# Performance work log

Measured on AMD Instinct MI355X. Metric: run time of the kernel, lower is better.

## Reference

```python
import jax, jax.numpy as jnp
import numpy as np

K = 3  # dynamic kernel size


def _conv(x, w, b, pad):
    # x: [B,Cin,H,W], w: [Cout,Cin,kh,kw]
    y = jax.lax.conv_general_dilated(
        x, w, window_strides=(1, 1), padding=pad,
        dimension_numbers=("NCHW", "OIHW", "NCHW"))
    return y + b[None, :, None, None]


def setup_inputs() -> dict:
    key = jax.random.key(0)
    ks = jax.random.split(key, 9)
    B, C, H, W = 16, 256, 64, 64
    sc1 = 1.0 / np.sqrt(C * 9)
    sc3 = 1.0 / np.sqrt(C)
    return {
        "x":    jax.random.normal(ks[0], (B, C, H, W), jnp.float32),
        "kin":  jax.random.normal(ks[1], (B, C, H, W), jnp.float32),
        "w1":   jax.random.normal(ks[2], (C, C, 3, 3), jnp.float32) * sc1,
        "b1":   jax.random.normal(ks[3], (C,), jnp.float32) * 0.01,
        "w2":   jax.random.normal(ks[4], (C, C, 3, 3), jnp.float32) * sc1,
        "b2":   jax.random.normal(ks[5], (C,), jnp.float32) * 0.01,
        "w3":   jax.random.normal(ks[6], (K * K * C, C, 1, 1), jnp.float32) * sc3,
        "b3":   jax.random.normal(ks[7], (K * K * C,), jnp.float32) * 0.01,
        "bias": jax.random.normal(ks[8], (C,), jnp.float32) * 0.01,
    }


def reference(x, kin, w1, b1, w2, b2, w3, b3, bias):
    B, C, H, W = x.shape
    # tokernel: conv3x3 (valid) -> lrelu(0.1) -> conv3x3 -> lrelu -> global avg pool -> 1x1 conv
    h = jax.nn.leaky_relu(_conv(kin, w1, b1, "VALID"), 0.1)
    h = jax.nn.leaky_relu(_conv(h, w2, b2, "VALID"), 0.1)
    p = h.mean(axis=(2, 3))                                   # [B,C] adaptive avg pool 1x1
    kern = jnp.einsum("bc,oc->bo", p, w3.reshape(K * K * C, C)) + b3  # 1x1 conv
    kern = kern.reshape(B, C, 1, K, K)                        # per-sample depthwise weights

    pad = [(K // 2, K // 2)] * 2

    def dw(xi, wi):  # xi: [C,H,W], wi: [C,1,K,K]
        return jax.lax.conv_general_dilated(
            xi[None], wi, window_strides=(1, 1), padding=pad,
            dimension_numbers=("NCHW", "OIHW", "NCHW"),
            feature_group_count=C)[0]

    y = jax.vmap(dw)(x, kern)                                 # [B,C,H,W]
    return y + bias[None, :, None, None]
```

## Files before the change

kernel.cpp:

```cpp
#include <hip/hip_runtime.h>
#include <hip/hip_bf16.h>
#include <stdint.h>

#define CCH 256

typedef __attribute__((ext_vector_type(8))) short short8;
typedef __attribute__((ext_vector_type(4))) float f32x4;

__device__ __forceinline__ float lrelu(float v) { return v > 0.f ? v : 0.1f * v; }

__device__ __forceinline__ unsigned short f2bf(float f) {
    __hip_bfloat16 h = __float2bfloat16(f);
    return *reinterpret_cast<unsigned short*>(&h);
}

__device__ __forceinline__ void gl_lds16(const void* g, void* s) {
    __builtin_amdgcn_global_load_lds(
        (const __attribute__((address_space(1))) unsigned int*)(uintptr_t)g,
        (__attribute__((address_space(3))) unsigned int*)(unsigned int)(uintptr_t)s,
        16, 0, 0);
}

__device__ __forceinline__ void pipe_barrier() {
    asm volatile("" ::: "memory");
    __builtin_amdgcn_s_barrier();
    asm volatile("" ::: "memory");
}

__global__ __launch_bounds__(256)
void nhwc_k(const float* __restrict__ in, unsigned short* __restrict__ out)
{
    __shared__ float t[32][65];
    const int tid = threadIdx.x;
    const int kc = blockIdx.x, y = blockIdx.y, b = blockIdx.z;
    const float* src = in + ((size_t)(b * 256 + kc * 32)) * 4096 + y * 64;
#pragma unroll
    for (int i = 0; i < 2; ++i) {
        int idx = tid + i * 256;
        int cl = idx >> 4, xg = idx & 15;
        float4 v = *(const float4*)(src + (size_t)cl * 4096 + xg * 4);
        t[cl][xg * 4 + 0] = v.x; t[cl][xg * 4 + 1] = v.y;
        t[cl][xg * 4 + 2] = v.z; t[cl][xg * 4 + 3] = v.w;
    }
    __syncthreads();
    const int x = tid >> 2, cg = tid & 3;
    union { unsigned short us[8]; uint4 v; } u;
#pragma unroll
    for (int j = 0; j < 8; ++j) u.us[j] = f2bf(t[cg * 8 + j][x]);
    unsigned short* dst = out + (((size_t)(b * 8 + kc) * 4096 + y * 64 + x) * 32 + cg * 8);
    *(uint4*)dst = u.v;
}

__global__ __launch_bounds__(256)
void wtr_k(const float* __restrict__ w1, const float* __restrict__ w2,
           unsigned short* __restrict__ o1, unsigned short* __restrict__ o2)
{
    const int kc = blockIdx.x / 9, t = blockIdx.x - kc * 9;
    const float* w = blockIdx.y ? w2 : w1;
    unsigned short* o = blockIdx.y ? o2 : o1;
    const int co = threadIdx.x;
#pragma unroll
    for (int q = 0; q < 4; ++q) {
        union { unsigned short us[8]; uint4 v; } u;
#pragma unroll
        for (int uu = 0; uu < 8; ++uu)
            u.us[uu] = f2bf(w[((size_t)co * 256 + kc * 32 + q * 8 + uu) * 9 + t]);
        *(uint4*)(o + ((size_t)((kc * 9 + t) * 4 + q)) * 2048 + co * 8) = u.v;
    }
}

__global__ __launch_bounds__(256)
void zero_pool_k(float* __restrict__ p) { p[blockIdx.x * 256 + threadIdx.x] = 0.f; }

template<int POOL, int WIN, int WOUT>
__global__ __launch_bounds__(256, 2)
void convmm_k(const unsigned short* __restrict__ im, const unsigned short* __restrict__ wt,
              const float* __restrict__ bias, unsigned short* __restrict__ outp,
              float* __restrict__ pool)
{
    constexpr int HINPIX = WIN * WIN;
    constexpr int NVAL   = WOUT * WOUT;
    constexpr int NB = 4 * 2056 + 4 * 1032;
    __shared__ __align__(16) short Ls[3 * NB];

    const int tid  = threadIdx.x;
    const int wave = tid >> 6;
    const int lane = tid & 63;
    const int quad = lane >> 4;
    const int l15  = lane & 15;
    const int wm   = (wave & 1) * 128;
    const int wn   = (wave >> 1) * 64;
    const int nb0  = blockIdx.x * 128;
    const int b    = blockIdx.y;

    const unsigned short* abase = wt + (size_t)wave * 2048 + (size_t)lane * 8;
    size_t bofs[2];
#pragma unroll
    for (int h = 0; h < 2; ++h) {
        int nn = nb0 + h * 64 + lane;
        if (nn > NVAL - 1) nn = NVAL - 1;
        int y = nn / WOUT, x = nn - y * WOUT;
        bofs[h] = ((size_t)(b * 8) * HINPIX + (size_t)y * WIN + x) * 32 + wave * 8;
    }

    f32x4 acc[8][4];
#pragma unroll
    for (int i = 0; i < 8; ++i)
#pragma unroll
        for (int j = 0; j < 4; ++j) { f32x4 z = {0.f, 0.f, 0.f, 0.f}; acc[i][j] = z; }

    auto stage = [&](int ss, short* buf) {
        const int kc = ss / 9, t = ss - kc * 9;
        const int ky = t / 3, kx = t - ky * 3;
        const size_t aoff = (size_t)ss * 8192;
        const size_t boff = ((size_t)kc * HINPIX + (size_t)ky * WIN + kx) * 32;
        short* al = buf + wave * 2056;
        short* bl = buf + 4 * 2056 + wave * 1032;
#pragma unroll
        for (int h = 0; h < 4; ++h)
            gl_lds16(abase + aoff + h * 512, al + h * 512);
#pragma unroll
        for (int h = 0; h < 2; ++h)
            gl_lds16(im + bofs[h] + boff, bl + h * 512);
    };

    auto compute = [&](const short* buf) {
        const short* ap = buf + quad * 2056;
        const short* bp = buf + 4 * 2056 + quad * 1032;
        short8 a[8], bfr[4];
#pragma unroll
        for (int i = 0; i < 8; ++i)
            a[i]  = *(const short8*)(ap + (wm + i * 16 + l15) * 8);
#pragma unroll
        for (int j = 0; j < 4; ++j)
            bfr[j] = *(const short8*)(bp + (wn + j * 16 + l15) * 8);
        __builtin_amdgcn_s_setprio(1);
#pragma unroll
        for (int i = 0; i < 8; ++i)
#pragma unroll
            for (int j = 0; j < 4; ++j)
                acc[i][j] = __builtin_amdgcn_mfma_f32_16x16x32_bf16(a[i], bfr[j], acc[i][j], 0, 0, 0);
        __builtin_amdgcn_s_setprio(0);
    };

    short* B0 = Ls;
    short* B1 = Ls + NB;
    short* B2 = Ls + 2 * NB;

    stage(0, B0);
    stage(1, B1);
    asm volatile("s_waitcnt vmcnt(6)" ::: "memory");
    pipe_barrier();

    short *c0 = B0, *c1 = B1, *c2 = B2;
    for (int s = 0; s < 70; ++s) {
        stage(s + 2, c2);
        compute(c0);
        asm volatile("s_waitcnt vmcnt(6)" ::: "memory");
        pipe_barrier();
        short* t = c0; c0 = c1; c1 = c2; c2 = t;
    }
    compute(c0);
    asm volatile("s_waitcnt vmcnt(0)" ::: "memory");
    pipe_barrier();
    compute(c1);

    const int co_l = wm + quad * 4;
    if (!POOL) {
#pragma unroll
        for (int i = 0; i < 8; ++i) {
            const int c0i = co_l + i * 16;
            float4 bv = *(const float4*)(bias + c0i);
            unsigned short* dstp = outp + ((size_t)(b * 8 + (c0i >> 5)) * NVAL) * 32 + (c0i & 31);
#pragma unroll
            for (int j = 0; j < 4; ++j) {
                int nn = nb0 + wn + j * 16 + l15;
                if (nn < NVAL) {
                    ushort4 pk = make_ushort4(
                        f2bf(lrelu(acc[i][j].x + bv.x)),
                        f2bf(lrelu(acc[i][j].y + bv.y)),
                        f2bf(lrelu(acc[i][j].z + bv.z)),
                        f2bf(lrelu(acc[i][j].w + bv.w)));
                    *(ushort4*)(dstp + (size_t)nn * 32) = pk;
                }
            }
        }
    } else {
#pragma unroll
        for (int i = 0; i < 8; ++i) {
            const int c0i = co_l + i * 16;
            float4 bv = *(const float4*)(bias + c0i);
            float s0 = 0.f, s1 = 0.f, s2 = 0.f, s3 = 0.f;
#pragma unroll
            for (int j = 0; j < 4; ++j) {
                int nn = nb0 + wn + j * 16 + l15;
                if (nn < NVAL) {
                    s0 += lrelu(acc[i][j].x + bv.x);
                    s1 += lrelu(acc[i][j].y + bv.y);
                    s2 += lrelu(acc[i][j].z + bv.z);
                    s3 += lrelu(acc[i][j].w + bv.w);
                }
            }
#pragma unroll
            for (int off = 1; off < 16; off <<= 1) {
                s0 += __shfl_xor(s0, off, 64);
                s1 += __shfl_xor(s1, off, 64);
                s2 += __shfl_xor(s2, off, 64);
                s3 += __shfl_xor(s3, off, 64);
            }
            if (l15 == 0) {
                float* pp = pool + b * 256 + c0i;
                atomicAdd(pp + 0, s0); atomicAdd(pp + 1, s1);
                atomicAdd(pp + 2, s2); atomicAdd(pp + 3, s3);
            }
        }
    }
}

__global__ __launch_bounds__(256)
void kern_gemm_k(const float* __restrict__ p, const float* __restrict__ w3,
                 const float* __restrict__ b3, float* __restrict__ kern)
{
    const int b = blockIdx.y;
    const int o = blockIdx.x * 256 + threadIdx.x;
    __shared__ float pv[CCH];
    pv[threadIdx.x] = p[b * CCH + threadIdx.x] * (1.f / 3600.f);
    __syncthreads();
    float acc = b3[o];
    const float* wr = w3 + (size_t)o * CCH;
#pragma unroll 4
    for (int c = 0; c < CCH; c += 4) {
        float4 wv = *(const float4*)(wr + c);
        acc += wv.x * pv[c] + wv.y * pv[c + 1] + wv.z * pv[c + 2] + wv.w * pv[c + 3];
    }
    kern[(size_t)b * (9 * CCH) + o] = acc;
}

__global__ __launch_bounds__(256)
void dw_k(const float* __restrict__ x, const float* __restrict__ kern,
          const float* __restrict__ bias, float* __restrict__ out)
{
    __shared__ float t[66 * 67];
    const int tid = threadIdx.x;
    const int bc = blockIdx.x;
    const int c = bc & (CCH - 1);
    const int b = bc >> 8;

#pragma unroll
    for (int i = 0; i < 18; ++i) {
        int idx = tid + i * 256;
        if (idx < 66 * 67) t[idx] = 0.f;
    }

    const float* kp = kern + (size_t)b * (9 * CCH) + c * 9;
    float k[9];
#pragma unroll
    for (int q = 0; q < 9; ++q) k[q] = kp[q];
    const float bs = bias[c];
    const float* xp = x + (size_t)bc * 4096;
    float* op = out + (size_t)bc * 4096;
    __syncthreads();

#pragma unroll
    for (int i = 0; i < 4; ++i) {
        int p4 = tid + i * 256;
        float4 v = *(const float4*)(xp + p4 * 4);
        int yy = p4 >> 4, xx = (p4 & 15) * 4;
        float* d = &t[(yy + 1) * 67 + 1 + xx];
        d[0] = v.x; d[1] = v.y; d[2] = v.z; d[3] = v.w;
    }
    __syncthreads();

#pragma unroll
    for (int i = 0; i < 4; ++i) {
        int p4 = tid + i * 256;
        int yy = p4 >> 4, xx = (p4 & 15) * 4;
        float r[3][6];
#pragma unroll
        for (int dy = 0; dy < 3; ++dy)
#pragma unroll
            for (int dx = 0; dx < 6; ++dx)
                r[dy][dx] = t[(yy + dy) * 67 + xx + dx];
        float4 o;
        float* ov = (float*)&o;
#pragma unroll
        for (int j = 0; j < 4; ++j) {
            float a = bs;
#pragma unroll
            for (int dy = 0; dy < 3; ++dy)
#pragma unroll
                for (int dx = 0; dx < 3; ++dx)
                    a += k[dy * 3 + dx] * r[dy][j + dx];
            ov[j] = a;
        }
        *(float4*)(op + p4 * 4) = o;
    }
}

extern "C" void kernel_launch(void* const* d_in, const int* in_sizes, int n_in,
                              void* d_out, int out_size, void* d_ws, size_t ws_size,
                              hipStream_t stream)
{
    const float* x    = (const float*)d_in[0];
    const float* kin  = (const float*)d_in[1];
    const float* w1   = (const float*)d_in[2];
    const float* b1   = (const float*)d_in[3];
    const float* w2   = (const float*)d_in[4];
    const float* b2   = (const float*)d_in[5];
    const float* w3   = (const float*)d_in[6];
    const float* b3   = (const float*)d_in[7];
    const float* bias = (const float*)d_in[8];

    unsigned short* imA = (unsigned short*)d_ws;
    unsigned short* h1  = imA + (size_t)16 * 8 * 4096 * 32;
    unsigned short* w1t = h1 + (size_t)16 * 8 * 3844 * 32 + 8192;
    unsigned short* w2t = w1t + (size_t)72 * 4 * 2048;
    float* pool = (float*)(w2t + (size_t)72 * 4 * 2048);
    float* kern = pool + 16 * 256;

    float* out = (float*)d_out;

    hipLaunchKernelGGL(zero_pool_k, dim3(16), dim3(256), 0, stream, pool);
    hipLaunchKernelGGL(nhwc_k, dim3(8, 64, 16), dim3(256), 0, stream, kin, imA);
    hipLaunchKernelGGL(wtr_k, dim3(72, 2), dim3(256), 0, stream, w1, w2, w1t, w2t);
    hipLaunchKernelGGL((convmm_k<0, 64, 62>), dim3(31, 16), dim3(256), 0, stream,
                       imA, w1t, b1, h1, (float*)nullptr);
    hipLaunchKernelGGL((convmm_k<1, 62, 60>), dim3(29, 16), dim3(256), 0, stream,
                       h1, w2t, b2, (unsigned short*)nullptr, pool);
    hipLaunchKernelGGL(kern_gemm_k, dim3(9, 16), dim3(256), 0, stream, pool, w3, b3, kern);
    hipLaunchKernelGGL(dw_k, dim3(16 * 256), dim3(256), 0, stream, x, kern, bias, out);
}
```

Measured before the change: 341.0 us.

## Enlarge conv GEMM tile to 256x256 using 32x32x16 MFMA

The implicit-GEMM conv kernels now use a 256-pixel N tile per block, with each wave computing 128x128 through 32x32x16 bf16 MFMAs in place of 16x16x32. This raises arithmetic intensity per LDS load and halves the number of blocks. In exchange the kernel runs at one block per CU with larger LDS buffers and more accumulator registers. With only 256 and 240 blocks on a chip with many CUs, occupancy and load balance may suffer.

```diff
diff --git a/kernel.cpp b/kernel.cpp
--- a/kernel.cpp
+++ b/kernel.cpp
@@ -6,6 +6,7 @@
 
 typedef __attribute__((ext_vector_type(8))) short short8;
 typedef __attribute__((ext_vector_type(4))) float f32x4;
+typedef __attribute__((ext_vector_type(16))) float f32x16;
 
 __device__ __forceinline__ float lrelu(float v) { return v > 0.f ? v : 0.1f * v; }
 
@@ -73,74 +74,83 @@
 void zero_pool_k(float* __restrict__ p) { p[blockIdx.x * 256 + threadIdx.x] = 0.f; }
 
 template<int POOL, int WIN, int WOUT>
-__global__ __launch_bounds__(256, 2)
+__global__ __launch_bounds__(256, 1)
 void convmm_k(const unsigned short* __restrict__ im, const unsigned short* __restrict__ wt,
               const float* __restrict__ bias, unsigned short* __restrict__ outp,
               float* __restrict__ pool)
 {
     constexpr int HINPIX = WIN * WIN;
     constexpr int NVAL   = WOUT * WOUT;
-    constexpr int NB = 4 * 2056 + 4 * 1032;
+    constexpr int PLS = 2056;
+    constexpr int NB  = 8 * PLS;
     __shared__ __align__(16) short Ls[3 * NB];
 
     const int tid  = threadIdx.x;
     const int wave = tid >> 6;
     const int lane = tid & 63;
-    const int quad = lane >> 4;
-    const int l15  = lane & 15;
+    const int l31  = lane & 31;
+    const int hi   = lane >> 5;
     const int wm   = (wave & 1) * 128;
-    const int wn   = (wave >> 1) * 64;
-    const int nb0  = blockIdx.x * 128;
+    const int wn   = (wave >> 1) * 128;
+    const int nb0  = blockIdx.x * 256;
     const int b    = blockIdx.y;
 
     const unsigned short* abase = wt + (size_t)wave * 2048 + (size_t)lane * 8;
-    size_t bofs[2];
-#pragma unroll
-    for (int h = 0; h < 2; ++h) {
+    size_t bofs[4];
+#pragma unroll
+    for (int h = 0; h < 4; ++h) {
         int nn = nb0 + h * 64 + lane;
         if (nn > NVAL - 1) nn = NVAL - 1;
         int y = nn / WOUT, x = nn - y * WOUT;
         bofs[h] = ((size_t)(b * 8) * HINPIX + (size_t)y * WIN + x) * 32 + wave * 8;
     }
 
-    f32x4 acc[8][4];
-#pragma unroll
-    for (int i = 0; i < 8; ++i)
-#pragma unroll
-        for (int j = 0; j < 4; ++j) { f32x4 z = {0.f, 0.f, 0.f, 0.f}; acc[i][j] = z; }
+    f32x16 acc[4][4];
+#pragma unroll
+    for (int i = 0; i < 4; ++i)
+#pragma unroll
+        for (int j = 0; j < 4; ++j)
+#pragma unroll
+            for (int e = 0; e < 16; ++e) acc[i][j][e] = 0.f;
 
     auto stage = [&](int ss, short* buf) {
         const int kc = ss / 9, t = ss - kc * 9;
         const int ky = t / 3, kx = t - ky * 3;
         const size_t aoff = (size_t)ss * 8192;
         const size_t boff = ((size_t)kc * HINPIX + (size_t)ky * WIN + kx) * 32;
-        short* al = buf + wave * 2056;
-        short* bl = buf + 4 * 2056 + wave * 1032;
+        short* al = buf + wave * PLS;
+        short* bl = buf + 4 * PLS + wave * PLS;
 #pragma unroll
         for (int h = 0; h < 4; ++h)
             gl_lds16(abase + aoff + h * 512, al + h * 512);
 #pragma unroll
-        for (int h = 0; h < 2; ++h)
+        for (int h = 0; h < 4; ++h)
             gl_lds16(im + bofs[h] + boff, bl + h * 512);
     };
 
     auto compute = [&](const short* buf) {
-        const short* ap = buf + quad * 2056;
-        const short* bp = buf + 4 * 2056 + quad * 1032;
-        short8 a[8], bfr[4];
-#pragma unroll
-        for (int i = 0; i < 8; ++i)
-            a[i]  = *(const short8*)(ap + (wm + i * 16 + l15) * 8);
-#pragma unroll
-        for (int j = 0; j < 4; ++j)
-            bfr[j] = *(const short8*)(bp + (wn + j * 16 + l15) * 8);
-        __builtin_amdgcn_s_setprio(1);
-#pragma unroll
-        for (int i = 0; i < 8; ++i)
-#pragma unroll
-            for (int j = 0; j < 4; ++j)
-                acc[i][j] = __builtin_amdgcn_mfma_f32_16x16x32_bf16(a[i], bfr[j], acc[i][j], 0, 0, 0);
-        __builtin_amdgcn_s_setprio(0);
+        const short* Ab = buf;
+        const short* Bb = buf + 4 * PLS;
+#pragma unroll
+        for (int kh = 0; kh < 2; ++kh) {
+            const short* ap = Ab + (kh * 2 + hi) * PLS;
+            const short* bp = Bb + (kh * 2 + hi) * PLS;
+            short8 a[4], bb[4];
+#pragma unroll
+            for (int mi = 0; mi < 4; ++mi)
+                a[mi] = *(const short8*)(ap + (wm + mi * 32 + l31) * 8);
+#pragma unroll
+            for (int nj = 0; nj < 4; ++nj)
+                bb[nj] = *(const short8*)(bp + (wn + nj * 32 + l31) * 8);
+            __builtin_amdgcn_s_setprio(1);
+#pragma unroll
+            for (int mi = 0; mi < 4; ++mi)
+#pragma unroll
+                for (int nj = 0; nj < 4; ++nj)
+                    acc[mi][nj] = __builtin_amdgcn_mfma_f32_32x32x16_bf16(
+                        a[mi], bb[nj], acc[mi][nj], 0, 0, 0);
+            __builtin_amdgcn_s_setprio(0);
+        }
     };
 
     short* B0 = Ls;
@@ -149,14 +159,14 @@
 
     stage(0, B0);
     stage(1, B1);
-    asm volatile("s_waitcnt vmcnt(6)" ::: "memory");
+    asm volatile("s_waitcnt vmcnt(8)" ::: "memory");
     pipe_barrier();
 
     short *c0 = B0, *c1 = B1, *c2 = B2;
     for (int s = 0; s < 70; ++s) {
         stage(s + 2, c2);
         compute(c0);
-        asm volatile("s_waitcnt vmcnt(6)" ::: "memory");
+        asm volatile("s_waitcnt vmcnt(8)" ::: "memory");
         pipe_barrier();
         short* t = c0; c0 = c1; c1 = c2; c2 = t;
     }
@@ -165,53 +175,67 @@
     pipe_barrier();
     compute(c1);
 
-    const int co_l = wm + quad * 4;
+    const int co_l = wm + 4 * hi;
     if (!POOL) {
 #pragma unroll
-        for (int i = 0; i < 8; ++i) {
-            const int c0i = co_l + i * 16;
-            float4 bv = *(const float4*)(bias + c0i);
-            unsigned short* dstp = outp + ((size_t)(b * 8 + (c0i >> 5)) * NVAL) * 32 + (c0i & 31);
-#pragma unroll
-            for (int j = 0; j < 4; ++j) {
-                int nn = nb0 + wn + j * 16 + l15;
+        for (int mi = 0; mi < 4; ++mi) {
+            const int kc = (wm >> 5) + mi;
+            float4 bv[4];
+#pragma unroll
+            for (int g = 0; g < 4; ++g)
+                bv[g] = *(const float4*)(bias + co_l + mi * 32 + 8 * g);
+            unsigned short* dstp = outp + ((size_t)(b * 8 + kc) * NVAL) * 32 + 4 * hi;
+#pragma unroll
+            for (int nj = 0; nj < 4; ++nj) {
+                int nn = nb0 + wn + nj * 32 + l31;
                 if (nn < NVAL) {
-                    ushort4 pk = make_ushort4(
-                        f2bf(lrelu(acc[i][j].x + bv.x)),
-                        f2bf(lrelu(acc[i][j].y + bv.y)),
-                        f2bf(lrelu(acc[i][j].z + bv.z)),
-                        f2bf(lrelu(acc[i][j].w + bv.w)));
-                    *(ushort4*)(dstp + (size_t)nn * 32) = pk;
+                    unsigned short* dq = dstp + (size_t)nn * 32;
+#pragma unroll
+                    for (int g = 0; g < 4; ++g) {
+                        ushort4 pk = make_ushort4(
+                            f2bf(lrelu(acc[mi][nj][g * 4 + 0] + bv[g].x)),
+                            f2bf(lrelu(acc[mi][nj][g * 4 + 1] + bv[g].y)),
+                            f2bf(lrelu(acc[mi][nj][g * 4 + 2] + bv[g].z)),
+                            f2bf(lrelu(acc[mi][nj][g * 4 + 3] + bv[g].w)));
+                        *(ushort4*)(dq + 8 * g) = pk;
+                    }
                 }
             }
         }
     } else {
 #pragma unroll
-        for (int i = 0; i < 8; ++i) {
-            const int c0i = co_l + i * 16;
-            float4 bv = *(const float4*)(bias + c0i);
-            float s0 = 0.f, s1 = 0.f, s2 = 0.f, s3 = 0.f;
-#pragma unroll
-            for (int j = 0; j < 4; ++j) {
-                int nn = nb0 + wn + j * 16 + l15;
+        for (int mi = 0; mi < 4; ++mi) {
+            float bb[16];
+#pragma unroll
+            for (int g = 0; g < 4; ++g) {
+                float4 v = *(const float4*)(bias + co_l + mi * 32 + 8 * g);
+                bb[g * 4 + 0] = v.x; bb[g * 4 + 1] = v.y;
+                bb[g * 4 + 2] = v.z; bb[g * 4 + 3] = v.w;
+            }
+            float s[16];
+#pragma unroll
+            for (int e = 0; e < 16; ++e) s[e] = 0.f;
+#pragma unroll
+            for (int nj = 0; nj < 4; ++nj) {
+                int nn = nb0 + wn + nj * 32 + l31;
                 if (nn < NVAL) {
-                    s0 += lrelu(acc[i][j].x + bv.x);
-                    s1 += lrelu(acc[i][j].y + bv.y);
-                    s2 += lrelu(acc[i][j].z + bv.z);
-                    s3 += lrelu(acc[i][j].w + bv.w);
+#pragma unroll
+                    for (int e = 0; e < 16; ++e)
+                        s[e] += lrelu(acc[mi][nj][e] + bb[e]);
                 }
             }
 #pragma unroll
-            for (int off = 1; off < 16; off <<= 1) {
-                s0 += __shfl_xor(s0, off, 64);
-                s1 += __shfl_xor(s1, off, 64);
-                s2 += __shfl_xor(s2, off, 64);
-                s3 += __shfl_xor(s3, off, 64);
-            }
-            if (l15 == 0) {
-                float* pp = pool + b * 256 + c0i;
-                atomicAdd(pp + 0, s0); atomicAdd(pp + 1, s1);
-                atomicAdd(pp + 2, s2); atomicAdd(pp + 3, s3);
+            for (int off = 1; off < 32; off <<= 1)
+#pragma unroll
+                for (int e = 0; e < 16; ++e)
+                    s[e] += __shfl_xor(s[e], off, 64);
+            if (l31 == 0) {
+                float* pp = pool + b * 256 + co_l + mi * 32;
+#pragma unroll
+                for (int g = 0; g < 4; ++g)
+#pragma unroll
+                    for (int r = 0; r < 4; ++r)
+                        atomicAdd(pp + 8 * g + r, s[g * 4 + r]);
             }
         }
     }
@@ -323,9 +347,9 @@
     hipLaunchKernelGGL(zero_pool_k, dim3(16), dim3(256), 0, stream, pool);
     hipLaunchKernelGGL(nhwc_k, dim3(8, 64, 16), dim3(256), 0, stream, kin, imA);
     hipLaunchKernelGGL(wtr_k, dim3(72, 2), dim3(256), 0, stream, w1, w2, w1t, w2t);
-    hipLaunchKernelGGL((convmm_k<0, 64, 62>), dim3(31, 16), dim3(256), 0, stream,
+    hipLaunchKernelGGL((convmm_k<0, 64, 62>), dim3(16, 16), dim3(256), 0, stream,
                        imA, w1t, b1, h1, (float*)nullptr);
-    hipLaunchKernelGGL((convmm_k<1, 62, 60>), dim3(29, 16), dim3(256), 0, stream,
+    hipLaunchKernelGGL((convmm_k<1, 62, 60>), dim3(15, 16), dim3(256), 0, stream,
                        h1, w2t, b2, (unsigned short*)nullptr, pool);
     hipLaunchKernelGGL(kern_gemm_k, dim3(9, 16), dim3(256), 0, stream, pool, w3, b3, kern);
     hipLaunchKernelGGL(dw_k, dim3(16 * 256), dim3(256), 0, stream, x, kern, bias, out);
```

After: 358.0 us. 1.05x slower.

## Reorder weight and activation LDS layout into MFMA fragment order

Applied to the files above, without the earlier changes.

Changes the pre-transposed weight layout and the LDS staging layout so each 16-row fragment chunk is stored contiguously in the order MFMA operands are read. Each lane then reads its short8 operand at lane*8 + i*512, a linear conflict-free pattern, instead of strided row addressing with padded rows. The global-to-LDS loads for the B operand are remapped to match: each wave now loads 16-pixel groups split by channel quad. The intent is to remove LDS bank conflicts and address arithmetic in the GEMM inner loop. In exchange the B global loads become less coalesced, since each lane reads 16 bytes from a 64-byte-strided pixel record.

```diff
diff --git a/kernel.cpp b/kernel.cpp
--- a/kernel.cpp
+++ b/kernel.cpp
@@ -55,17 +55,21 @@
 void wtr_k(const float* __restrict__ w1, const float* __restrict__ w2,
            unsigned short* __restrict__ o1, unsigned short* __restrict__ o2)
 {
-    const int kc = blockIdx.x / 9, t = blockIdx.x - kc * 9;
+    const int ss = blockIdx.x;
+    const int kc = ss / 9, t = ss - kc * 9;
     const float* w = blockIdx.y ? w2 : w1;
     unsigned short* o = blockIdx.y ? o2 : o1;
-    const int co = threadIdx.x;
-#pragma unroll
-    for (int q = 0; q < 4; ++q) {
+#pragma unroll
+    for (int rep = 0; rep < 4; ++rep) {
+        int slot = threadIdx.x + rep * 256;
+        int f = slot >> 6, l = slot & 63;
+        int co = f * 16 + (l & 15);
+        int q  = l >> 4;
         union { unsigned short us[8]; uint4 v; } u;
 #pragma unroll
         for (int uu = 0; uu < 8; ++uu)
             u.us[uu] = f2bf(w[((size_t)co * 256 + kc * 32 + q * 8 + uu) * 9 + t]);
-        *(uint4*)(o + ((size_t)((kc * 9 + t) * 4 + q)) * 2048 + co * 8) = u.v;
+        *(uint4*)(o + (size_t)ss * 8192 + slot * 8) = u.v;
     }
 }
 
@@ -80,7 +84,7 @@
 {
     constexpr int HINPIX = WIN * WIN;
     constexpr int NVAL   = WOUT * WOUT;
-    constexpr int NB = 4 * 2056 + 4 * 1032;
+    constexpr int NB = 16 * 512 + 8 * 512;
     __shared__ __align__(16) short Ls[3 * NB];
 
     const int tid  = threadIdx.x;
@@ -93,14 +97,14 @@
     const int nb0  = blockIdx.x * 128;
     const int b    = blockIdx.y;
 
-    const unsigned short* abase = wt + (size_t)wave * 2048 + (size_t)lane * 8;
+    const unsigned short* abase = wt + (size_t)(wave * 4) * 512 + (size_t)lane * 8;
     size_t bofs[2];
 #pragma unroll
     for (int h = 0; h < 2; ++h) {
-        int nn = nb0 + h * 64 + lane;
+        int nn = nb0 + (wave * 2 + h) * 16 + l15;
         if (nn > NVAL - 1) nn = NVAL - 1;
         int y = nn / WOUT, x = nn - y * WOUT;
-        bofs[h] = ((size_t)(b * 8) * HINPIX + (size_t)y * WIN + x) * 32 + wave * 8;
+        bofs[h] = ((size_t)(b * 8) * HINPIX + (size_t)y * WIN + x) * 32 + quad * 8;
     }
 
     f32x4 acc[8][4];
@@ -114,26 +118,25 @@
         const int ky = t / 3, kx = t - ky * 3;
         const size_t aoff = (size_t)ss * 8192;
         const size_t boff = ((size_t)kc * HINPIX + (size_t)ky * WIN + kx) * 32;
-        short* al = buf + wave * 2056;
-        short* bl = buf + 4 * 2056 + wave * 1032;
+        short* bl = buf + 16 * 512;
 #pragma unroll
         for (int h = 0; h < 4; ++h)
-            gl_lds16(abase + aoff + h * 512, al + h * 512);
+            gl_lds16(abase + aoff + h * 512, buf + (wave * 4 + h) * 512);
 #pragma unroll
         for (int h = 0; h < 2; ++h)
-            gl_lds16(im + bofs[h] + boff, bl + h * 512);
+            gl_lds16(im + bofs[h] + boff, bl + (wave * 2 + h) * 512);
     };
 
     auto compute = [&](const short* buf) {
-        const short* ap = buf + quad * 2056;
-        const short* bp = buf + 4 * 2056 + quad * 1032;
+        const short* ap = buf + (size_t)(wave & 1) * 8 * 512 + lane * 8;
+        const short* bp = buf + 16 * 512 + (size_t)(wave >> 1) * 4 * 512 + lane * 8;
         short8 a[8], bfr[4];
 #pragma unroll
         for (int i = 0; i < 8; ++i)
-            a[i]  = *(const short8*)(ap + (wm + i * 16 + l15) * 8);
+            a[i]  = *(const short8*)(ap + i * 512);
 #pragma unroll
         for (int j = 0; j < 4; ++j)
-            bfr[j] = *(const short8*)(bp + (wn + j * 16 + l15) * 8);
+            bfr[j] = *(const short8*)(bp + j * 512);
         __builtin_amdgcn_s_setprio(1);
 #pragma unroll
         for (int i = 0; i < 8; ++i)
@@ -314,8 +317,8 @@
     unsigned short* imA = (unsigned short*)d_ws;
     unsigned short* h1  = imA + (size_t)16 * 8 * 4096 * 32;
     unsigned short* w1t = h1 + (size_t)16 * 8 * 3844 * 32 + 8192;
-    unsigned short* w2t = w1t + (size_t)72 * 4 * 2048;
-    float* pool = (float*)(w2t + (size_t)72 * 4 * 2048);
+    unsigned short* w2t = w1t + (size_t)72 * 8192;
+    float* pool = (float*)(w2t + (size_t)72 * 8192);
     float* kern = pool + 16 * 256;
 
     float* out = (float*)d_out;
```

Result: faster. 332.6 us (-2.5%).
